# Kernel tuning notes

Hardware: AMD Instinct MI355X
Metric: run time of the kernel (lower is better)

The kernel has to match this reference:

```python
import jax, jax.numpy as jnp
import numpy as np

E = 64          # moe_num_experts
H = 1024        # hidden_size
F = 2816        # per_expert_ff_dim
T = 4096        # total tokens (equal split: 64 per expert)


def setup_inputs() -> dict:
    key = jax.random.key(0)
    k1, k2, k3, k4 = jax.random.split(key, 4)
    s = 1.0 / np.sqrt(H)
    return {
        "x": jax.random.normal(k1, (T, H), dtype=jnp.float32),
        "tokens_per_expert": jnp.full((E,), T // E, dtype=jnp.int32),
        "w1": jax.random.normal(k2, (E * F, H), dtype=jnp.float32) * s,
        "w3": jax.random.normal(k3, (E * F, H), dtype=jnp.float32) * s,
        "w2": jax.random.normal(k4, (E * F, H), dtype=jnp.float32) * s,
    }


def reference(x, tokens_per_expert, w1, w3, w2):
    # Tokens are grouped contiguously per expert with an equal split,
    # so the variable-size grouped GEMM (gg.ops.gmm) reduces to a batched einsum.
    tpe = x.shape[0] // E
    xg = x.reshape(E, tpe, H)            # [E, t, h]
    w1e = w1.reshape(E, F, H)
    w3e = w3.reshape(E, F, H)
    w2e = w2.reshape(E, F, H)
    # gmm(x, w1, trans_b=True): per-expert x @ w1[e].T
    h1 = jnp.einsum("eth,efh->etf", xg, w1e)   # [E, t, f]
    h3 = jnp.einsum("eth,efh->etf", xg, w3e)   # [E, t, f]
    gated = jax.nn.silu(h1) * h3               # SwiGLU
    # gmm(gated, w2): per-expert gated @ w2[e]  ([t,f] @ [f,h])
    out = jnp.einsum("etf,efh->eth", gated, w2e)
    return out.reshape(-1, H)
```

## Files before the change

### kernel.cpp

```cpp
#include <hip/hip_runtime.h>
#include <hip/hip_bf16.h>

#define NE   64
#define NH   1024
#define NF   2816
#define TPE  64
#define BK   64
#define PITCH 72

typedef __attribute__((ext_vector_type(8))) short bf16x8;
typedef __attribute__((ext_vector_type(4))) float f32x4;

__device__ __forceinline__ ushort f2bf(float f) {
    union { float f; unsigned u; } v; v.f = f;
    unsigned r = v.u + 0x7fffu + ((v.u >> 16) & 1u);
    return (ushort)(r >> 16);
}

__device__ __forceinline__ bf16x8 cvt8(f32x4 lo, f32x4 hi) {
    bf16x8 r;
    #pragma unroll
    for (int j = 0; j < 4; ++j) {
        r[j]     = (short)f2bf(lo[j]);
        r[4 + j] = (short)f2bf(hi[j]);
    }
    return r;
}

#define GLOAD16(gsrc, ldst)                                                          \
    __builtin_amdgcn_global_load_lds(                                                \
        (const __attribute__((address_space(1))) void*)(gsrc),                       \
        (__attribute__((address_space(3))) void*)(ldst), 16, 0, 0)

__global__ __launch_bounds__(256, 3)
void k1_gate(const float* __restrict__ x,
             const float* __restrict__ w1,
             const float* __restrict__ w3,
             ushort* __restrict__ g) {
    __shared__ float lA [64 * 64];
    __shared__ float lB1[64 * 64];
    __shared__ float lB3[64 * 64];

    const int jt   = blockIdx.x;
    const int e    = blockIdx.y;
    const int tid  = threadIdx.x;
    const int lane = tid & 63;
    const int wid  = tid >> 6;
    const int m15  = lane & 15;
    const int hi   = lane >> 4;

    const float* xA = x  + (size_t)e * TPE * NH;
    const float* B1 = w1 + ((size_t)e * NF + (size_t)jt * 64) * NH;
    const float* B3 = w3 + ((size_t)e * NF + (size_t)jt * 64) * NH;

    f32x4 acc1[4], acc3[4];
    #pragma unroll
    for (int nf = 0; nf < 4; ++nf) {
        acc1[nf] = f32x4{0.f, 0.f, 0.f, 0.f};
        acc3[nf] = f32x4{0.f, 0.f, 0.f, 0.f};
    }

    const int mrow = wid * 16 + m15;

    for (int kt = 0; kt < NH / BK; ++kt) {
        __syncthreads();
        #pragma unroll
        for (int r = 0; r < 4; ++r) {
            const int s    = r * 256 + tid;
            const int row  = s >> 4;
            const int c16  = (s & 15) ^ (row & 15);
            const size_t goff = (size_t)row * NH + (size_t)kt * BK + c16 * 4;
            const int lbase = (s & ~63) * 4;
            GLOAD16(xA + goff, lA  + lbase);
            GLOAD16(B1 + goff, lB1 + lbase);
            GLOAD16(B3 + goff, lB3 + lbase);
        }
        __syncthreads();

        #pragma unroll
        for (int ks = 0; ks < 2; ++ks) {
            const int c0 = ks * 8 + hi * 2;
            const int sa0 = (c0    ) ^ m15;
            const int sa1 = (c0 + 1) ^ m15;
            const f32x4 a0 = *(const f32x4*)&lA[mrow * 64 + sa0 * 4];
            const f32x4 a1 = *(const f32x4*)&lA[mrow * 64 + sa1 * 4];
            const bf16x8 af = cvt8(a0, a1);
            #pragma unroll
            for (int nf = 0; nf < 4; ++nf) {
                const int brow = nf * 16 + m15;
                const f32x4 p0 = *(const f32x4*)&lB1[brow * 64 + sa0 * 4];
                const f32x4 p1 = *(const f32x4*)&lB1[brow * 64 + sa1 * 4];
                acc1[nf] = __builtin_amdgcn_mfma_f32_16x16x32_bf16(af, cvt8(p0, p1), acc1[nf], 0, 0, 0);
                const f32x4 q0 = *(const f32x4*)&lB3[brow * 64 + sa0 * 4];
                const f32x4 q1 = *(const f32x4*)&lB3[brow * 64 + sa1 * 4];
                acc3[nf] = __builtin_amdgcn_mfma_f32_16x16x32_bf16(af, cvt8(q0, q1), acc3[nf], 0, 0, 0);
            }
        }
    }

    #pragma unroll
    for (int nf = 0; nf < 4; ++nf) {
        #pragma unroll
        for (int i = 0; i < 4; ++i) {
            const float h1v = acc1[nf][i];
            const float h3v = acc3[nf][i];
            const float s   = (h1v / (1.f + __expf(-h1v))) * h3v;
            const int row = wid * 16 + (hi * 4) + i;
            const int col = jt * 64 + nf * 16 + m15;
            const size_t t = (size_t)e * TPE + row;
            g[t * NF + col] = f2bf(s);
        }
    }
}

__global__ __launch_bounds__(256, 2)
void k2_down(const ushort* __restrict__ g,
             const float* __restrict__ w2,
             float* __restrict__ out) {
    __shared__ ushort lA[64 * PITCH];
    __shared__ ushort lB[64 * PITCH];

    const int jt   = blockIdx.x;
    const int e    = blockIdx.y;
    const int tid  = threadIdx.x;
    const int lane = tid & 63;
    const int wid  = tid >> 6;

    const ushort* A = g  + (size_t)e * TPE * NF;
    const float*  B = w2 + (size_t)e * NF * NH + (size_t)jt * 64;
    float* O = out + (size_t)e * TPE * NH + (size_t)jt * 64;

    f32x4 acc[4];
    for (int nf = 0; nf < 4; ++nf) acc[nf] = f32x4{0.f, 0.f, 0.f, 0.f};

    for (int kt = 0; kt < NF / BK; ++kt) {
        __syncthreads();
        #pragma unroll
        for (int r = 0; r < 2; ++r) {
            const int q   = tid + r * 256;
            const int row = q >> 3;
            const int k8  = (q & 7) * 8;
            *(bf16x8*)(&lA[row * PITCH + k8]) =
                *(const bf16x8*)(A + (size_t)row * NF + kt * BK + k8);
        }
        {
            const int n  = tid & 63;
            const int kq = (tid >> 6) * 4;
            #pragma unroll
            for (int r = 0; r < 4; ++r) {
                const int ks = kq + r * 16;
                const size_t base = (size_t)(kt * BK + ks) * NH + n;
                const float f0 = B[base];
                const float f1 = B[base + NH];
                const float f2 = B[base + 2 * (size_t)NH];
                const float f3 = B[base + 3 * (size_t)NH];
                ushort4 b;
                b.x = f2bf(f0); b.y = f2bf(f1); b.z = f2bf(f2); b.w = f2bf(f3);
                *(ushort4*)(&lB[n * PITCH + ks]) = b;
            }
        }
        __syncthreads();

        const int mrow = wid * 16 + (lane & 15);
        #pragma unroll
        for (int ks = 0; ks < 2; ++ks) {
            const int koff = ks * 32 + ((lane >> 4) * 8);
            const bf16x8 af = *(const bf16x8*)(&lA[mrow * PITCH + koff]);
            #pragma unroll
            for (int nf = 0; nf < 4; ++nf) {
                const bf16x8 bfr = *(const bf16x8*)(&lB[(nf * 16 + (lane & 15)) * PITCH + koff]);
                acc[nf] = __builtin_amdgcn_mfma_f32_16x16x32_bf16(af, bfr, acc[nf], 0, 0, 0);
            }
        }
    }

    #pragma unroll
    for (int nf = 0; nf < 4; ++nf) {
        #pragma unroll
        for (int i = 0; i < 4; ++i) {
            const int row = wid * 16 + ((lane >> 4) * 4) + i;
            const int col = nf * 16 + (lane & 15);
            O[(size_t)row * NH + col] = acc[nf][i];
        }
    }
}

extern "C" void kernel_launch(void* const* d_in, const int* in_sizes, int n_in,
                              void* d_out, int out_size, void* d_ws, size_t ws_size,
                              hipStream_t stream) {
    const float* x  = (const float*)d_in[0];
    const float* w1 = (const float*)d_in[2];
    const float* w3 = (const float*)d_in[3];
    const float* w2 = (const float*)d_in[4];
    float* out = (float*)d_out;
    ushort* gated = (ushort*)d_ws;

    dim3 g1(NF / 64, NE);
    k1_gate<<<g1, dim3(256), 0, stream>>>(x, w1, w3, gated);

    dim3 g2(NH / 64, NE);
    k2_down<<<g2, dim3(256), 0, stream>>>(gated, w2, out);
}
```

Measured before the change: 440.6 us.

## Double-buffer k1 LDS with register prefetch and convert to bf16 before staging

The gate kernel no longer uses direct global-to-LDS fp32 loads. It prefetches the next K tile into registers, converts it to bf16, and writes it into a second LDS buffer while MFMAs run on the current one. This halves LDS footprint and read traffic, drops the repeated per-wave conversions, and replaces two barriers per iteration with one. The cost is 48 extra VGPRs for prefetch, which may hurt the 3-block occupancy target, plus one redundant load on the last iteration.

```diff
diff --git a/kernel.cpp b/kernel.cpp
--- a/kernel.cpp
+++ b/kernel.cpp
@@ -7,6 +7,7 @@
 #define TPE  64
 #define BK   64
 #define PITCH 72
+#define K1BUF 12288
 
 typedef __attribute__((ext_vector_type(8))) short bf16x8;
 typedef __attribute__((ext_vector_type(4))) float f32x4;
@@ -26,20 +27,13 @@
     }
     return r;
 }
-
-#define GLOAD16(gsrc, ldst)                                                          \
-    __builtin_amdgcn_global_load_lds(                                                \
-        (const __attribute__((address_space(1))) void*)(gsrc),                       \
-        (__attribute__((address_space(3))) void*)(ldst), 16, 0, 0)
 
 __global__ __launch_bounds__(256, 3)
 void k1_gate(const float* __restrict__ x,
              const float* __restrict__ w1,
              const float* __restrict__ w3,
              ushort* __restrict__ g) {
-    __shared__ float lA [64 * 64];
-    __shared__ float lB1[64 * 64];
-    __shared__ float lB3[64 * 64];
+    __shared__ ushort lds[2 * K1BUF];
 
     const int jt   = blockIdx.x;
     const int e    = blockIdx.y;
@@ -48,11 +42,20 @@
     const int wid  = tid >> 6;
     const int m15  = lane & 15;
     const int hi   = lane >> 4;
+    const int mrow = wid * 16 + m15;
 
     const float* xA = x  + (size_t)e * TPE * NH;
     const float* B1 = w1 + ((size_t)e * NF + (size_t)jt * 64) * NH;
     const float* B3 = w3 + ((size_t)e * NF + (size_t)jt * 64) * NH;
 
+    const int row0 = tid >> 3;
+    const int c80  = tid & 7;
+    const int row1 = row0 + 32;
+    const int wo0  = row0 * 64 + ((c80 ^ (row0 & 7)) << 3);
+    const int wo1  = row1 * 64 + ((c80 ^ (row1 & 7)) << 3);
+    const size_t go0 = (size_t)row0 * NH + c80 * 8;
+    const size_t go1 = (size_t)row1 * NH + c80 * 8;
+
     f32x4 acc1[4], acc3[4];
     #pragma unroll
     for (int nf = 0; nf < 4; ++nf) {
@@ -60,43 +63,64 @@
         acc3[nf] = f32x4{0.f, 0.f, 0.f, 0.f};
     }
 
-    const int mrow = wid * 16 + m15;
+    f32x4 r[12];
+    #define ISSUE_LOADS(kt)                                                     \
+        do {                                                                    \
+            const size_t kb = (size_t)(kt) * BK;                                \
+            r[0]  = *(const f32x4*)(xA + go0 + kb);                             \
+            r[1]  = *(const f32x4*)(xA + go0 + kb + 4);                         \
+            r[2]  = *(const f32x4*)(xA + go1 + kb);                             \
+            r[3]  = *(const f32x4*)(xA + go1 + kb + 4);                         \
+            r[4]  = *(const f32x4*)(B1 + go0 + kb);                             \
+            r[5]  = *(const f32x4*)(B1 + go0 + kb + 4);                         \
+            r[6]  = *(const f32x4*)(B1 + go1 + kb);                             \
+            r[7]  = *(const f32x4*)(B1 + go1 + kb + 4);                         \
+            r[8]  = *(const f32x4*)(B3 + go0 + kb);                             \
+            r[9]  = *(const f32x4*)(B3 + go0 + kb + 4);                         \
+            r[10] = *(const f32x4*)(B3 + go1 + kb);                             \
+            r[11] = *(const f32x4*)(B3 + go1 + kb + 4);                         \
+        } while (0)
+
+    #define WRITE_STAGE(buf)                                                    \
+        do {                                                                    \
+            *(bf16x8*)((buf) + wo0)            = cvt8(r[0],  r[1]);             \
+            *(bf16x8*)((buf) + wo1)            = cvt8(r[2],  r[3]);             \
+            *(bf16x8*)((buf) + 4096 + wo0)     = cvt8(r[4],  r[5]);             \
+            *(bf16x8*)((buf) + 4096 + wo1)     = cvt8(r[6],  r[7]);             \
+            *(bf16x8*)((buf) + 8192 + wo0)     = cvt8(r[8],  r[9]);             \
+            *(bf16x8*)((buf) + 8192 + wo1)     = cvt8(r[10], r[11]);            \
+        } while (0)
+
+    ISSUE_LOADS(0);
+    WRITE_STAGE(lds);
+    __syncthreads();
 
     for (int kt = 0; kt < NH / BK; ++kt) {
-        __syncthreads();
-        #pragma unroll
-        for (int r = 0; r < 4; ++r) {
-            const int s    = r * 256 + tid;
-            const int row  = s >> 4;
-            const int c16  = (s & 15) ^ (row & 15);
-            const size_t goff = (size_t)row * NH + (size_t)kt * BK + c16 * 4;
-            const int lbase = (s & ~63) * 4;
-            GLOAD16(xA + goff, lA  + lbase);
-            GLOAD16(B1 + goff, lB1 + lbase);
-            GLOAD16(B3 + goff, lB3 + lbase);
-        }
-        __syncthreads();
-
+        const int ktn = (kt + 1 < NH / BK) ? kt + 1 : NH / BK - 1;
+        ISSUE_LOADS(ktn);
+
+        const ushort* rb = lds + (kt & 1) * K1BUF;
         #pragma unroll
         for (int ks = 0; ks < 2; ++ks) {
-            const int c0 = ks * 8 + hi * 2;
-            const int sa0 = (c0    ) ^ m15;
-            const int sa1 = (c0 + 1) ^ m15;
-            const f32x4 a0 = *(const f32x4*)&lA[mrow * 64 + sa0 * 4];
-            const f32x4 a1 = *(const f32x4*)&lA[mrow * 64 + sa1 * 4];
-            const bf16x8 af = cvt8(a0, a1);
+            const int sa = ((ks * 4 + hi) ^ (mrow & 7)) << 3;
+            const bf16x8 af = *(const bf16x8*)(rb + mrow * 64 + sa);
             #pragma unroll
             for (int nf = 0; nf < 4; ++nf) {
                 const int brow = nf * 16 + m15;
-                const f32x4 p0 = *(const f32x4*)&lB1[brow * 64 + sa0 * 4];
-                const f32x4 p1 = *(const f32x4*)&lB1[brow * 64 + sa1 * 4];
-                acc1[nf] = __builtin_amdgcn_mfma_f32_16x16x32_bf16(af, cvt8(p0, p1), acc1[nf], 0, 0, 0);
-                const f32x4 q0 = *(const f32x4*)&lB3[brow * 64 + sa0 * 4];
-                const f32x4 q1 = *(const f32x4*)&lB3[brow * 64 + sa1 * 4];
-                acc3[nf] = __builtin_amdgcn_mfma_f32_16x16x32_bf16(af, cvt8(q0, q1), acc3[nf], 0, 0, 0);
+                const int sb = ((ks * 4 + hi) ^ (brow & 7)) << 3;
+                const bf16x8 b1 = *(const bf16x8*)(rb + 4096 + brow * 64 + sb);
+                acc1[nf] = __builtin_amdgcn_mfma_f32_16x16x32_bf16(af, b1, acc1[nf], 0, 0, 0);
+                const bf16x8 b3 = *(const bf16x8*)(rb + 8192 + brow * 64 + sb);
+                acc3[nf] = __builtin_amdgcn_mfma_f32_16x16x32_bf16(af, b3, acc3[nf], 0, 0, 0);
             }
         }
-    }
+
+        ushort* wb = lds + ((kt + 1) & 1) * K1BUF;
+        WRITE_STAGE(wb);
+        __syncthreads();
+    }
+    #undef ISSUE_LOADS
+    #undef WRITE_STAGE
 
     #pragma unroll
     for (int nf = 0; nf < 4; ++nf) {
```

New measurement: 495.3 us. 12.4% more time.

## Widen gate kernel N-tile to 128, halve K-step, reorder grid expert-major

Applied to the files above, without the earlier changes.

The gate/up kernel now computes 128 output columns per block instead of 64, so each x tile loaded into LDS is reused across twice as many weight rows. The K step shrinks from 64 to 32 so the LDS footprint stays small, with an 8-chunk XOR swizzle, and the launch bound rises to 4 blocks per CU. The grid is reordered with the expert on blockIdx.x. The aim is less redundant x traffic and more occupancy, at the cost of twice as many accumulator registers and twice as many barrier-separated K iterations.

```diff
diff --git a/kernel.cpp b/kernel.cpp
--- a/kernel.cpp
+++ b/kernel.cpp
@@ -5,7 +5,6 @@
 #define NH   1024
 #define NF   2816
 #define TPE  64
-#define BK   64
 #define PITCH 72
 
 typedef __attribute__((ext_vector_type(8))) short bf16x8;
@@ -32,81 +31,84 @@
         (const __attribute__((address_space(1))) void*)(gsrc),                       \
         (__attribute__((address_space(3))) void*)(ldst), 16, 0, 0)
 
-__global__ __launch_bounds__(256, 3)
+__global__ __launch_bounds__(256, 4)
 void k1_gate(const float* __restrict__ x,
              const float* __restrict__ w1,
              const float* __restrict__ w3,
              ushort* __restrict__ g) {
-    __shared__ float lA [64 * 64];
-    __shared__ float lB1[64 * 64];
-    __shared__ float lB3[64 * 64];
-
-    const int jt   = blockIdx.x;
-    const int e    = blockIdx.y;
+    __shared__ float lds[10240];
+    float* lX  = lds;
+    float* lW1 = lds + 2048;
+    float* lW3 = lds + 6144;
+
+    const int e    = blockIdx.x;
+    const int jtt  = blockIdx.y;
     const int tid  = threadIdx.x;
     const int lane = tid & 63;
     const int wid  = tid >> 6;
     const int m15  = lane & 15;
     const int hi   = lane >> 4;
+    const int mrow = wid * 16 + m15;
 
     const float* xA = x  + (size_t)e * TPE * NH;
-    const float* B1 = w1 + ((size_t)e * NF + (size_t)jt * 64) * NH;
-    const float* B3 = w3 + ((size_t)e * NF + (size_t)jt * 64) * NH;
-
-    f32x4 acc1[4], acc3[4];
-    #pragma unroll
-    for (int nf = 0; nf < 4; ++nf) {
+    const float* B1 = w1 + ((size_t)e * NF + (size_t)jtt * 128) * NH;
+    const float* B3 = w3 + ((size_t)e * NF + (size_t)jtt * 128) * NH;
+
+    f32x4 acc1[8], acc3[8];
+    #pragma unroll
+    for (int nf = 0; nf < 8; ++nf) {
         acc1[nf] = f32x4{0.f, 0.f, 0.f, 0.f};
         acc3[nf] = f32x4{0.f, 0.f, 0.f, 0.f};
     }
 
-    const int mrow = wid * 16 + m15;
-
-    for (int kt = 0; kt < NH / BK; ++kt) {
-        __syncthreads();
-        #pragma unroll
-        for (int r = 0; r < 4; ++r) {
-            const int s    = r * 256 + tid;
-            const int row  = s >> 4;
-            const int c16  = (s & 15) ^ (row & 15);
-            const size_t goff = (size_t)row * NH + (size_t)kt * BK + c16 * 4;
-            const int lbase = (s & ~63) * 4;
-            GLOAD16(xA + goff, lA  + lbase);
-            GLOAD16(B1 + goff, lB1 + lbase);
-            GLOAD16(B3 + goff, lB3 + lbase);
-        }
-        __syncthreads();
-
-        #pragma unroll
-        for (int ks = 0; ks < 2; ++ks) {
-            const int c0 = ks * 8 + hi * 2;
-            const int sa0 = (c0    ) ^ m15;
-            const int sa1 = (c0 + 1) ^ m15;
-            const f32x4 a0 = *(const f32x4*)&lA[mrow * 64 + sa0 * 4];
-            const f32x4 a1 = *(const f32x4*)&lA[mrow * 64 + sa1 * 4];
-            const bf16x8 af = cvt8(a0, a1);
-            #pragma unroll
-            for (int nf = 0; nf < 4; ++nf) {
-                const int brow = nf * 16 + m15;
-                const f32x4 p0 = *(const f32x4*)&lB1[brow * 64 + sa0 * 4];
-                const f32x4 p1 = *(const f32x4*)&lB1[brow * 64 + sa1 * 4];
-                acc1[nf] = __builtin_amdgcn_mfma_f32_16x16x32_bf16(af, cvt8(p0, p1), acc1[nf], 0, 0, 0);
-                const f32x4 q0 = *(const f32x4*)&lB3[brow * 64 + sa0 * 4];
-                const f32x4 q1 = *(const f32x4*)&lB3[brow * 64 + sa1 * 4];
-                acc3[nf] = __builtin_amdgcn_mfma_f32_16x16x32_bf16(af, cvt8(q0, q1), acc3[nf], 0, 0, 0);
-            }
-        }
-    }
-
-    #pragma unroll
-    for (int nf = 0; nf < 4; ++nf) {
+    const int s0 = (2 * hi) ^ (m15 & 7);
+    const int s1 = s0 ^ 1;
+
+    for (int kt = 0; kt < NH / 32; ++kt) {
+        const size_t kb = (size_t)kt * 32;
+        __syncthreads();
+        #pragma unroll
+        for (int i = 0; i < 2; ++i) {
+            const int S   = i * 256 + tid;
+            const int row = S >> 3;
+            const int cs  = (S & 7) ^ (row & 7);
+            GLOAD16(xA + (size_t)row * NH + kb + cs * 4, lX + (S & ~63) * 4);
+        }
+        #pragma unroll
+        for (int i = 0; i < 4; ++i) {
+            const int S   = i * 256 + tid;
+            const int row = S >> 3;
+            const int cs  = (S & 7) ^ (row & 7);
+            const size_t goff = (size_t)row * NH + kb + cs * 4;
+            GLOAD16(B1 + goff, lW1 + (S & ~63) * 4);
+            GLOAD16(B3 + goff, lW3 + (S & ~63) * 4);
+        }
+        __syncthreads();
+
+        const f32x4 a0 = *(const f32x4*)&lX[mrow * 32 + s0 * 4];
+        const f32x4 a1 = *(const f32x4*)&lX[mrow * 32 + s1 * 4];
+        const bf16x8 af = cvt8(a0, a1);
+        #pragma unroll
+        for (int nf = 0; nf < 8; ++nf) {
+            const int brow = nf * 16 + m15;
+            const f32x4 p0 = *(const f32x4*)&lW1[brow * 32 + s0 * 4];
+            const f32x4 p1 = *(const f32x4*)&lW1[brow * 32 + s1 * 4];
+            acc1[nf] = __builtin_amdgcn_mfma_f32_16x16x32_bf16(af, cvt8(p0, p1), acc1[nf], 0, 0, 0);
+            const f32x4 q0 = *(const f32x4*)&lW3[brow * 32 + s0 * 4];
+            const f32x4 q1 = *(const f32x4*)&lW3[brow * 32 + s1 * 4];
+            acc3[nf] = __builtin_amdgcn_mfma_f32_16x16x32_bf16(af, cvt8(q0, q1), acc3[nf], 0, 0, 0);
+        }
+    }
+
+    #pragma unroll
+    for (int nf = 0; nf < 8; ++nf) {
         #pragma unroll
         for (int i = 0; i < 4; ++i) {
             const float h1v = acc1[nf][i];
             const float h3v = acc3[nf][i];
             const float s   = (h1v / (1.f + __expf(-h1v))) * h3v;
             const int row = wid * 16 + (hi * 4) + i;
-            const int col = jt * 64 + nf * 16 + m15;
+            const int col = jtt * 128 + nf * 16 + m15;
             const size_t t = (size_t)e * TPE + row;
             g[t * NF + col] = f2bf(s);
         }
@@ -133,7 +135,7 @@
     f32x4 acc[4];
     for (int nf = 0; nf < 4; ++nf) acc[nf] = f32x4{0.f, 0.f, 0.f, 0.f};
 
-    for (int kt = 0; kt < NF / BK; ++kt) {
+    for (int kt = 0; kt < NF / 64; ++kt) {
         __syncthreads();
         #pragma unroll
         for (int r = 0; r < 2; ++r) {
@@ -141,7 +143,7 @@
             const int row = q >> 3;
             const int k8  = (q & 7) * 8;
             *(bf16x8*)(&lA[row * PITCH + k8]) =
-                *(const bf16x8*)(A + (size_t)row * NF + kt * BK + k8);
+                *(const bf16x8*)(A + (size_t)row * NF + kt * 64 + k8);
         }
         {
             const int n  = tid & 63;
@@ -149,7 +151,7 @@
             #pragma unroll
             for (int r = 0; r < 4; ++r) {
                 const int ks = kq + r * 16;
-                const size_t base = (size_t)(kt * BK + ks) * NH + n;
+                const size_t base = (size_t)(kt * 64 + ks) * NH + n;
                 const float f0 = B[base];
                 const float f1 = B[base + NH];
                 const float f2 = B[base + 2 * (size_t)NH];
@@ -195,7 +197,7 @@
     float* out = (float*)d_out;
     ushort* gated = (ushort*)d_ws;
 
-    dim3 g1(NF / 64, NE);
+    dim3 g1(NE, NF / 128);
     k1_gate<<<g1, dim3(256), 0, stream>>>(x, w1, w3, gated);
 
     dim3 g2(NH / 64, NE);
```

Measured after the change: 489.5 us. 1.11x slower.
